# Kernel tuning notes

Measured on AMD Instinct MI355X. Metric: run time of the kernel, lower is better.

Reference implementation:

```python
import jax, jax.numpy as jnp
import numpy as np
from functools import partial

B, S, H = 1, 2048, 1024
F, E, K = 2048, 8, 2


def setup_inputs() -> dict:
    key = jax.random.key(0)
    ks = jax.random.split(key, 7)
    x = jax.random.normal(ks[0], (B, S, H), dtype=jnp.float32)
    weights = jax.random.uniform(ks[1], (B * S, E), dtype=jnp.float32)
    top_weights = jax.random.uniform(ks[2], (B * S, K), dtype=jnp.float32)
    top_experts = jax.random.randint(ks[3], (B * S, K), 0, E).astype(jnp.int64)
    scale = 0.02  # keep activations in a sane range
    w1 = jax.random.normal(ks[4], (E, F, H), dtype=jnp.float32) * scale
    v1 = jax.random.normal(ks[5], (E, F, H), dtype=jnp.float32) * scale
    w2 = jax.random.normal(ks[6], (E, F, H), dtype=jnp.float32) * scale
    return {"x": x, "weights": weights, "top_weights": top_weights,
            "top_experts": top_experts, "w1": w1, "v1": v1, "w2": w2}


def _moe_forward(x, top_weights, top_experts, w1, v1, w2):
    b, s, h = x.shape
    xf = x.reshape(-1, h)  # [T, H]
    n_exp = w1.shape[0]
    # combine weight per (token, expert): sum over top-k slots routed to e
    onehot = jax.nn.one_hot(top_experts, n_exp, dtype=x.dtype)      # [T, K, E]
    cw = jnp.einsum('tk,tke->et', top_weights, onehot)              # [E, T]

    def body(acc, inputs):
        w1e, v1e, w2e, cwe = inputs  # [F,H], [F,H], [F,H], [T]
        gate = jax.nn.silu(xf @ w1e.T)       # [T, F]
        inter = gate * (xf @ v1e.T)          # GLU
        down = inter @ w2e                   # [T, H]
        return acc + cwe[:, None] * down, None

    out, _ = jax.lax.scan(body, jnp.zeros_like(xf), (w1, v1, w2, cw))
    return out.reshape(b, s, h)


def reference(x, weights, top_weights, top_experts, w1, v1, w2):
    # `weights` (full router probs) is accepted but unused, as in the original.
    return _moe_forward(x, top_weights, top_experts, w1, v1, w2)
```

## Files before the change

kernel.cpp:

```cpp
#include <hip/hip_runtime.h>
#include <hip/hip_bf16.h>


#define T_ 2048
#define H_ 1024
#define F_ 2048
#define E_ 8

#define SCAP 768
#define NSLOT (E_ * SCAP)
#define MAXT2 (NSLOT / 128)

typedef unsigned short u16;
typedef short s8v __attribute__((ext_vector_type(8)));
typedef float f4v __attribute__((ext_vector_type(4)));
typedef unsigned short u16x4 __attribute__((ext_vector_type(4)));

__device__ __forceinline__ u16 f2bf(float f) {
    union { float f; unsigned u; } v; v.f = f;
    unsigned r = v.u + 0x7FFF + ((v.u >> 16) & 1);
    return (u16)(r >> 16);
}
__device__ __forceinline__ unsigned pkbf(float a, float b) {
    __hip_bfloat162 h = __float22bfloat162_rn(make_float2(a, b));
    union { __hip_bfloat162 h; unsigned u; } c; c.h = h; return c.u;
}
__device__ __forceinline__ int4 cvt8(const float4 a, const float4 b) {
    int4 r; r.x = (int)pkbf(a.x, a.y); r.y = (int)pkbf(a.z, a.w);
    r.z = (int)pkbf(b.x, b.y); r.w = (int)pkbf(b.z, b.w); return r;
}
__device__ __forceinline__ void async16(void* lds, const void* g) {
    __builtin_amdgcn_global_load_lds(
        (const __attribute__((address_space(1))) unsigned*)g,
        (__attribute__((address_space(3))) unsigned*)lds, 16, 0, 0);
}

__global__ void router_kernel(const int* __restrict__ te, const float* __restrict__ tw,
                              int* __restrict__ slot_tok, float* __restrict__ slot_w,
                              int* __restrict__ tok_slot,
                              int* __restrict__ tile_e, int* __restrict__ tile_s,
                              int* __restrict__ ntiles) {
    __shared__ int cnt[E_];
    __shared__ int s_any;
    int tid = threadIdx.x;
    if (tid < E_) cnt[tid] = 0;
    if (tid == 0) s_any = 0;
    __syncthreads();
    int any = 0;
    for (int i = tid; i < 2 * T_; i += 256) if (i & 1) any |= te[i];
    if (any) atomicOr(&s_any, 1);
    __syncthreads();
    bool is32 = (s_any != 0);
    for (int t = tid; t < T_; t += 256) {
        int e0 = is32 ? te[2 * t]     : te[4 * t];
        int e1 = is32 ? te[2 * t + 1] : te[4 * t + 2];
        float w0 = tw[2 * t], w1 = tw[2 * t + 1];
        if (e0 == e1) {
            int p = atomicAdd(&cnt[e0], 1);
            int s = (p < SCAP) ? e0 * SCAP + p : -1;
            if (s >= 0) { slot_tok[s] = t; slot_w[s] = w0 + w1; }
            tok_slot[2 * t] = s; tok_slot[2 * t + 1] = -1;
        } else {
            int p = atomicAdd(&cnt[e0], 1);
            int s = (p < SCAP) ? e0 * SCAP + p : -1;
            if (s >= 0) { slot_tok[s] = t; slot_w[s] = w0; }
            tok_slot[2 * t] = s;
            p = atomicAdd(&cnt[e1], 1);
            s = (p < SCAP) ? e1 * SCAP + p : -1;
            if (s >= 0) { slot_tok[s] = t; slot_w[s] = w1; }
            tok_slot[2 * t + 1] = s;
        }
    }
    __syncthreads();
    for (int e = 0; e < E_; ++e) {
        int c = min(cnt[e], SCAP);
        int pc = min((c + 127) & ~127, SCAP);
        for (int p = c + tid; p < pc; p += 256) {
            slot_tok[e * SCAP + p] = -1; slot_w[e * SCAP + p] = 0.f;
        }
    }
    __syncthreads();
    if (tid == 0) {
        int nt = 0;
        for (int e = 0; e < E_; ++e) {
            int pc = min((min(cnt[e], SCAP) + 127) & ~127, SCAP);
            for (int s = 0; s < pc; s += 128) { tile_e[nt] = e; tile_s[nt] = e * SCAP + s; ++nt; }
        }
        *ntiles = nt;
    }
}

__global__ void cvtwv_kernel(const float* __restrict__ w1, const float* __restrict__ v1,
                             u16* __restrict__ w1b, u16* __restrict__ v1b) {
    const float* src = blockIdx.y ? v1 : w1;
    u16* dst = blockIdx.y ? v1b : w1b;
    int i = (blockIdx.x * 256 + threadIdx.x) * 8;
    float4 a = *(const float4*)(src + i);
    float4 b = *(const float4*)(src + i + 4);
    *(int4*)(dst + i) = cvt8(a, b);
}

__global__ void tcvt8_kernel(const float* __restrict__ src0, u16* __restrict__ dst0) {
    const float* src = src0 + (size_t)blockIdx.z * F_ * H_;
    u16* dst = dst0 + (size_t)blockIdx.z * H_ * F_;
    __shared__ __align__(16) u16 tile[64][72];
    int bc = blockIdx.x * 64, br = blockIdx.y * 64;
    int tx = threadIdx.x, ty = threadIdx.y;
    for (int r = ty; r < 64; r += 32) {
        const float* p = src + (size_t)(br + r) * H_ + bc + tx * 8;
        float4 v0 = *(const float4*)p;
        float4 v1 = *(const float4*)(p + 4);
        u16* q = &tile[r][tx * 8];
        q[0] = f2bf(v0.x); q[1] = f2bf(v0.y); q[2] = f2bf(v0.z); q[3] = f2bf(v0.w);
        q[4] = f2bf(v1.x); q[5] = f2bf(v1.y); q[6] = f2bf(v1.z); q[7] = f2bf(v1.w);
    }
    __syncthreads();
    for (int c = ty; c < 64; c += 32) {
        u16 tmp[8];
#pragma unroll
        for (int j = 0; j < 8; ++j) tmp[j] = tile[tx * 8 + j][c];
        *(int4*)&dst[(size_t)(bc + c) * F_ + br + tx * 8] = *(int4*)tmp;
    }
}

__global__ void gather_x_kernel(const float* __restrict__ x, const int* __restrict__ slot_tok,
                                const int* __restrict__ tile_s, const int* __restrict__ ntiles,
                                u16* __restrict__ xg) {
    if ((int)blockIdx.x >= *ntiles) return;
    int base = tile_s[blockIdx.x];
    int tid = threadIdx.x;
    __shared__ int stok[128];
    if (tid < 128) stok[tid] = slot_tok[base + tid];
    __syncthreads();
    int c0 = blockIdx.y * 2048;
    for (int c = c0 + tid; c < c0 + 2048; c += 256) {
        int r = c >> 7, co = (c & 127) * 8;
        int tok = stok[r];
        u16* dst = xg + ((size_t)(base + r) << 10) + co;
        if (tok < 0) { *(int4*)dst = make_int4(0, 0, 0, 0); }
        else {
            const float* p = x + ((size_t)tok << 10) + co;
            *(int4*)dst = cvt8(*(const float4*)p, *(const float4*)(p + 4));
        }
    }
}

__global__ __launch_bounds__(256, 4) void glu_async_kernel(
        const u16* __restrict__ xg, const u16* __restrict__ w1b,
        const u16* __restrict__ v1b, const int* __restrict__ tile_e,
        const int* __restrict__ tile_s, const int* __restrict__ ntiles,
        const float* __restrict__ slot_w, u16* __restrict__ inter) {
    int bt = blockIdx.y;
    if (bt >= *ntiles) return;
    int e = tile_e[bt], s0 = tile_s[bt];
    int f0 = blockIdx.x * 64;
    __shared__ __align__(16) u16 As[2][128 * 32];
    __shared__ __align__(16) u16 B1s[2][64 * 32];
    __shared__ __align__(16) u16 B2s[2][64 * 32];
    __shared__ float swv[128];
    int tid = threadIdx.x;
    int lane = tid & 63, wave = tid >> 6;
    int wm = wave >> 1, wn = wave & 1;
    int ml = lane & 15, q = lane >> 4;
    if (tid < 128) swv[tid] = slot_w[s0 + tid];

    int row0 = (wave << 4) + (lane >> 2);
    int row1 = row0 + 64;
    int cs = ((lane & 3) ^ ((row0 >> 1) & 3)) << 3;
    const u16* gA0  = xg + ((size_t)(s0 + row0) << 10) + cs;
    const u16* gA1  = xg + ((size_t)(s0 + row1) << 10) + cs;
    const size_t wofs = (size_t)e * F_ * H_;
    const u16* gB1 = w1b + wofs + ((size_t)(f0 + row0) << 10) + cs;
    const u16* gB2 = v1b + wofs + ((size_t)(f0 + row0) << 10) + cs;
    int l0 = (row0 << 5) + ((lane & 3) << 3);
    int l1 = (row1 << 5) + ((lane & 3) << 3);
    int xs = (q ^ ((lane >> 1) & 3)) << 3;

    f4v accg[4][2] = {};
    f4v accu[4][2] = {};

    async16(&As[0][l0],  gA0);
    async16(&As[0][l1],  gA1);
    async16(&B1s[0][l0], gB1);
    async16(&B2s[0][l0], gB2);

    int cur = 0;
    for (int k0 = 0; k0 < H_; k0 += 32) {
        __syncthreads();
        if (k0 + 32 < H_) {
            int nx = cur ^ 1;
            async16(&As[nx][l0],  gA0 + k0 + 32);
            async16(&As[nx][l1],  gA1 + k0 + 32);
            async16(&B1s[nx][l0], gB1 + k0 + 32);
            async16(&B2s[nx][l0], gB2 + k0 + 32);
        }
        s8v a[4], b1[2], b2[2];
#pragma unroll
        for (int i = 0; i < 4; ++i)
            a[i]  = *(const s8v*)(&As[cur][(wm * 64 + i * 16 + ml) * 32 + xs]);
#pragma unroll
        for (int j = 0; j < 2; ++j) {
            b1[j] = *(const s8v*)(&B1s[cur][(wn * 32 + j * 16 + ml) * 32 + xs]);
            b2[j] = *(const s8v*)(&B2s[cur][(wn * 32 + j * 16 + ml) * 32 + xs]);
        }
#pragma unroll
        for (int i = 0; i < 4; ++i)
#pragma unroll
            for (int j = 0; j < 2; ++j) {
                accg[i][j] = __builtin_amdgcn_mfma_f32_16x16x32_bf16(a[i], b1[j], accg[i][j], 0, 0, 0);
                accu[i][j] = __builtin_amdgcn_mfma_f32_16x16x32_bf16(a[i], b2[j], accu[i][j], 0, 0, 0);
            }
        cur ^= 1;
    }
#pragma unroll
    for (int i = 0; i < 4; ++i)
#pragma unroll
        for (int r = 0; r < 4; ++r) {
            int lr = wm * 64 + i * 16 + q * 4 + r;
            float cv = swv[lr];
#pragma unroll
            for (int j = 0; j < 2; ++j) {
                float g = accg[i][j][r];
                float u = accu[i][j][r];
                float s = g / (1.f + __expf(-g));
                int f = f0 + wn * 32 + j * 16 + ml;
                inter[((size_t)(s0 + lr) << 11) + f] = f2bf(cv * s * u);
            }
        }
}

__global__ __launch_bounds__(256, 4) void down_async_kernel(
        const u16* __restrict__ inter, const u16* __restrict__ w2bT,
        const int* __restrict__ tile_e, const int* __restrict__ tile_s,
        const int* __restrict__ ntiles,
        float* __restrict__ dbufA, float* __restrict__ dbufB) {
    int bt = blockIdx.y;
    if (bt >= *ntiles) return;
    int e = tile_e[bt], s0 = tile_s[bt];
    int h0 = blockIdx.x * 64;
    int ks = blockIdx.z;
    int kbeg = ks * (F_ / 2);
    float* dbuf = ks ? dbufB : dbufA;
    __shared__ __align__(16) u16 As[2][128 * 32];
    __shared__ __align__(16) u16 Bs[2][64 * 32];
    int tid = threadIdx.x;
    int lane = tid & 63, wave = tid >> 6;
    int wm = wave >> 1, wn = wave & 1;
    int ml = lane & 15, q = lane >> 4;

    int row0 = (wave << 4) + (lane >> 2);
    int row1 = row0 + 64;
    int cs = ((lane & 3) ^ ((row0 >> 1) & 3)) << 3;
    const u16* gA0 = inter + ((size_t)(s0 + row0) << 11) + kbeg + cs;
    const u16* gA1 = inter + ((size_t)(s0 + row1) << 11) + kbeg + cs;
    const u16* gB  = w2bT + (size_t)e * H_ * F_ + ((size_t)(h0 + row0) << 11) + kbeg + cs;
    int l0 = (row0 << 5) + ((lane & 3) << 3);
    int l1 = (row1 << 5) + ((lane & 3) << 3);
    int xs = (q ^ ((lane >> 1) & 3)) << 3;

    f4v acc[4][2] = {};

    async16(&As[0][l0], gA0);
    async16(&As[0][l1], gA1);
    async16(&Bs[0][l0], gB);

    int cur = 0;
    for (int k0 = 0; k0 < F_ / 2; k0 += 32) {
        __syncthreads();
        if (k0 + 32 < F_ / 2) {
            int nx = cur ^ 1;
            async16(&As[nx][l0], gA0 + k0 + 32);
            async16(&As[nx][l1], gA1 + k0 + 32);
            async16(&Bs[nx][l0], gB  + k0 + 32);
        }
        s8v a[4], b[2];
#pragma unroll
        for (int i = 0; i < 4; ++i)
            a[i] = *(const s8v*)(&As[cur][(wm * 64 + i * 16 + ml) * 32 + xs]);
#pragma unroll
        for (int j = 0; j < 2; ++j)
            b[j] = *(const s8v*)(&Bs[cur][(wn * 32 + j * 16 + ml) * 32 + xs]);
#pragma unroll
        for (int i = 0; i < 4; ++i)
#pragma unroll
            for (int j = 0; j < 2; ++j)
                acc[i][j] = __builtin_amdgcn_mfma_f32_16x16x32_bf16(a[i], b[j], acc[i][j], 0, 0, 0);
        cur ^= 1;
    }
#pragma unroll
    for (int i = 0; i < 4; ++i)
#pragma unroll
        for (int r = 0; r < 4; ++r) {
            int lr = wm * 64 + i * 16 + q * 4 + r;
            float* drow = dbuf + ((size_t)(s0 + lr) << 10);
#pragma unroll
            for (int j = 0; j < 2; ++j) {
                int h = h0 + wn * 32 + j * 16 + ml;
                drow[h] = acc[i][j][r];
            }
        }
}

__global__ void combine_kernel(const float* __restrict__ dbufA, const float* __restrict__ dbufB,
                               const int* __restrict__ tok_slot, float* __restrict__ out) {
    int t = blockIdx.x;
    int c = threadIdx.x * 4;
    int s0 = tok_slot[2 * t], s1 = tok_slot[2 * t + 1];
    float4 acc = make_float4(0.f, 0.f, 0.f, 0.f);
    if (s0 >= 0) {
        float4 a = *(const float4*)(dbufA + ((size_t)s0 << 10) + c);
        float4 b = *(const float4*)(dbufB + ((size_t)s0 << 10) + c);
        acc.x = a.x + b.x; acc.y = a.y + b.y; acc.z = a.z + b.z; acc.w = a.w + b.w;
    }
    if (s1 >= 0) {
        float4 a = *(const float4*)(dbufA + ((size_t)s1 << 10) + c);
        float4 b = *(const float4*)(dbufB + ((size_t)s1 << 10) + c);
        acc.x += a.x + b.x; acc.y += a.y + b.y; acc.z += a.z + b.z; acc.w += a.w + b.w;
    }
    *(float4*)(out + ((size_t)t << 10) + c) = acc;
}

#define SCAP3 1024
__global__ void router3_kernel(const int* __restrict__ te, const float* __restrict__ tw,
                               int* __restrict__ cnt_g, int* __restrict__ slot_tok,
                               float* __restrict__ slot_w) {
    __shared__ int cnt[E_];
    __shared__ int s_any;
    int tid = threadIdx.x;
    if (tid < E_) cnt[tid] = 0;
    if (tid == 0) s_any = 0;
    __syncthreads();
    int any = 0;
    for (int i = tid; i < 2 * T_; i += 256) if (i & 1) any |= te[i];
    if (any) atomicOr(&s_any, 1);
    __syncthreads();
    bool is32 = (s_any != 0);
    for (int t = tid; t < T_; t += 256) {
        int e0 = is32 ? te[2 * t]     : te[4 * t];
        int e1 = is32 ? te[2 * t + 1] : te[4 * t + 2];
        float w0 = tw[2 * t], w1 = tw[2 * t + 1];
        if (e0 == e1) {
            int p = atomicAdd(&cnt[e0], 1);
            if (p < SCAP3) { slot_tok[e0 * SCAP3 + p] = t; slot_w[e0 * SCAP3 + p] = w0 + w1; }
        } else {
            int p = atomicAdd(&cnt[e0], 1);
            if (p < SCAP3) { slot_tok[e0 * SCAP3 + p] = t; slot_w[e0 * SCAP3 + p] = w0; }
            p = atomicAdd(&cnt[e1], 1);
            if (p < SCAP3) { slot_tok[e1 * SCAP3 + p] = t; slot_w[e1 * SCAP3 + p] = w1; }
        }
    }
    __syncthreads();
    for (int e = 0; e < E_; ++e) {
        int c = min(cnt[e], SCAP3);
        int pc = min((c + 127) & ~127, SCAP3);
        for (int p = c + tid; p < pc; p += 256) {
            slot_tok[e * SCAP3 + p] = 0; slot_w[e * SCAP3 + p] = 0.f;
        }
    }
    if (tid < E_) cnt_g[tid] = min(cnt[tid], SCAP3);
}
__global__ void cvt_kernel(const float* __restrict__ src, u16* __restrict__ dst) {
    int i = (blockIdx.x * 256 + threadIdx.x) * 4;
    float4 v = *(const float4*)(src + i);
    u16x4 o = { f2bf(v.x), f2bf(v.y), f2bf(v.z), f2bf(v.w) };
    *(u16x4*)(dst + i) = o;
}
__global__ __launch_bounds__(256, 2) void glu3_kernel(
        const u16* __restrict__ xb, const float* __restrict__ w1,
        const float* __restrict__ v1, const int* __restrict__ cnt_g,
        const int* __restrict__ slot_tok, const float* __restrict__ slot_w,
        u16* __restrict__ inter) {
    int e = blockIdx.x >> 3, tt = blockIdx.x & 7;
    if (tt * 128 >= cnt_g[e]) return;
    __shared__ __align__(16) u16 As[128 * 32];
    __shared__ __align__(16) u16 B1s[128 * 32];
    __shared__ __align__(16) u16 B2s[128 * 32];
    __shared__ int stok[128];
    __shared__ float sw[128];
    int tid = threadIdx.x;
    if (tid < 128) {
        stok[tid] = slot_tok[e * SCAP3 + tt * 128 + tid];
        sw[tid]   = slot_w[e * SCAP3 + tt * 128 + tid];
    }
    __syncthreads();
    int lane = tid & 63, wave = tid >> 6;
    int wm = wave >> 1, wn = wave & 1;
    int f0 = blockIdx.y * 128;
    int ml = lane & 15, q = lane >> 4;
    int r0 = tid >> 2, r1 = 64 + (tid >> 2);
    int colo = (tid & 3) * 8;
    const size_t tokoff0 = (size_t)stok[r0] * H_ + colo;
    const size_t tokoff1 = (size_t)stok[r1] * H_ + colo;
    const float* gb1 = w1 + (size_t)e * F_ * H_ + (size_t)f0 * H_;
    const float* gb2 = v1 + (size_t)e * F_ * H_ + (size_t)f0 * H_;
    const size_t boff0 = (size_t)r0 * H_ + colo;
    const size_t boff1 = (size_t)r1 * H_ + colo;
    f4v accg[4][4] = {};
    f4v accu[4][4] = {};
    for (int k0 = 0; k0 < H_; k0 += 32) {
        __syncthreads();
        *(int4*)(As + tid * 8)         = *(const int4*)(xb + tokoff0 + k0);
        *(int4*)(As + (256 + tid) * 8) = *(const int4*)(xb + tokoff1 + k0);
        const float* p = gb1 + boff0 + k0;
        *(int4*)(B1s + tid * 8) = cvt8(*(const float4*)p, *(const float4*)(p + 4));
        p = gb1 + boff1 + k0;
        *(int4*)(B1s + (256 + tid) * 8) = cvt8(*(const float4*)p, *(const float4*)(p + 4));
        p = gb2 + boff0 + k0;
        *(int4*)(B2s + tid * 8) = cvt8(*(const float4*)p, *(const float4*)(p + 4));
        p = gb2 + boff1 + k0;
        *(int4*)(B2s + (256 + tid) * 8) = cvt8(*(const float4*)p, *(const float4*)(p + 4));
        __syncthreads();
        s8v a[4], b1[4], b2[4];
#pragma unroll
        for (int i = 0; i < 4; ++i) {
            a[i]  = *(const s8v*)(As  + (wm * 64 + i * 16 + ml) * 32 + q * 8);
            b1[i] = *(const s8v*)(B1s + (wn * 64 + i * 16 + ml) * 32 + q * 8);
            b2[i] = *(const s8v*)(B2s + (wn * 64 + i * 16 + ml) * 32 + q * 8);
        }
#pragma unroll
        for (int i = 0; i < 4; ++i)
#pragma unroll
            for (int j = 0; j < 4; ++j) {
                accg[i][j] = __builtin_amdgcn_mfma_f32_16x16x32_bf16(a[i], b1[j], accg[i][j], 0, 0, 0);
                accu[i][j] = __builtin_amdgcn_mfma_f32_16x16x32_bf16(a[i], b2[j], accu[i][j], 0, 0, 0);
            }
    }
#pragma unroll
    for (int i = 0; i < 4; ++i)
#pragma unroll
        for (int r = 0; r < 4; ++r) {
            int lr = wm * 64 + i * 16 + q * 4 + r;
            float cv = sw[lr];
#pragma unroll
            for (int j = 0; j < 4; ++j) {
                float g = accg[i][j][r];
                float u = accu[i][j][r];
                float s = g / (1.f + __expf(-g));
                int f = f0 + wn * 64 + j * 16 + ml;
                inter[(size_t)(e * SCAP3 + tt * 128 + lr) * F_ + f] = f2bf(cv * s * u);
            }
        }
}
__global__ __launch_bounds__(256) void down3_kernel(
        const u16* __restrict__ inter, const u16* __restrict__ w2bT,
        const int* __restrict__ cnt_g, const int* __restrict__ slot_tok,
        float* __restrict__ out) {
    int e = blockIdx.x >> 3, tt = blockIdx.x & 7;
    if (tt * 128 >= cnt_g[e]) return;
    __shared__ __align__(16) u16 As[128 * 32];
    __shared__ __align__(16) u16 Bs[128 * 32];
    __shared__ int stok[128];
    int tid = threadIdx.x;
    if (tid < 128) stok[tid] = slot_tok[e * SCAP3 + tt * 128 + tid];
    __syncthreads();
    int lane = tid & 63, wave = tid >> 6;
    int wm = wave >> 1, wn = wave & 1;
    int h0 = blockIdx.y * 128;
    int ml = lane & 15, q = lane >> 4;
    int kbeg = blockIdx.z * (F_ / 2), kend = kbeg + (F_ / 2);
    f4v acc[4][4] = {};
    const u16* ga = inter + (size_t)(e * SCAP3 + tt * 128) * F_;
    const u16* gb = w2bT + (size_t)e * H_ * F_ + (size_t)h0 * F_;
    for (int k0 = kbeg; k0 < kend; k0 += 32) {
        __syncthreads();
#pragma unroll
        for (int p = 0; p < 2; ++p) {
            int c = p * 256 + tid;
            int r = c >> 2, co = (c & 3) * 8;
            *(int4*)(As + c * 8) = *(const int4*)(ga + (size_t)r * F_ + k0 + co);
            *(int4*)(Bs + c * 8) = *(const int4*)(gb + (size_t)r * F_ + k0 + co);
        }
        __syncthreads();
        s8v a[4], b[4];
#pragma unroll
        for (int i = 0; i < 4; ++i) {
            a[i] = *(const s8v*)(As + (wm * 64 + i * 16 + ml) * 32 + q * 8);
            b[i] = *(const s8v*)(Bs + (wn * 64 + i * 16 + ml) * 32 + q * 8);
        }
#pragma unroll
        for (int i = 0; i < 4; ++i)
#pragma unroll
            for (int j = 0; j < 4; ++j)
                acc[i][j] = __builtin_amdgcn_mfma_f32_16x16x32_bf16(a[i], b[j], acc[i][j], 0, 0, 0);
    }
#pragma unroll
    for (int i = 0; i < 4; ++i)
#pragma unroll
        for (int r = 0; r < 4; ++r) {
            int lr = wm * 64 + i * 16 + q * 4 + r;
            size_t trow = (size_t)stok[lr] * H_;
#pragma unroll
            for (int j = 0; j < 4; ++j) {
                int h = h0 + wn * 64 + j * 16 + ml;
                atomicAdd(&out[trow + h], acc[i][j][r]);
            }
        }
}

extern "C" void kernel_launch(void* const* d_in, const int* in_sizes, int n_in,
                              void* d_out, int out_size, void* d_ws, size_t ws_size,
                              hipStream_t stream) {
    const float* x  = (const float*)d_in[0];
    const float* tw = (const float*)d_in[2];
    const int*   te = (const int*)d_in[3];
    const float* w1 = (const float*)d_in[4];
    const float* v1 = (const float*)d_in[5];
    const float* w2 = (const float*)d_in[6];
    float* out = (float*)d_out;
    char* ws = (char*)d_ws;

    if (ws_size >= ((size_t)135 << 20)) {
        int*   ntiles   = (int*)(ws);
        int*   tile_e   = (int*)(ws + 256);
        int*   tile_s   = (int*)(ws + 512);
        int*   tok_slot = (int*)(ws + (4 << 10));
        int*   slot_tok = (int*)(ws + (20 << 10));
        float* slot_w   = (float*)(ws + (44 << 10));
        u16*   xg       = (u16*)(ws + ((size_t)1 << 20));
        u16*   w1b      = (u16*)(ws + ((size_t)13 << 20));
        u16*   v1b      = (u16*)(ws + ((size_t)45 << 20));
        u16*   w2bT     = (u16*)(ws + ((size_t)77 << 20));
        u16*   inter    = (u16*)(ws + ((size_t)109 << 20));
        float* dbufA    = (float*)(ws + ((size_t)13 << 20));
        float* dbufB    = (float*)(ws + ((size_t)45 << 20));

        router_kernel<<<1, 256, 0, stream>>>(te, tw, slot_tok, slot_w, tok_slot,
                                             tile_e, tile_s, ntiles);
        cvtwv_kernel<<<dim3((E_ * F_ * H_) / 2048, 2), 256, 0, stream>>>(w1, v1, w1b, v1b);
        tcvt8_kernel<<<dim3(H_ / 64, F_ / 64, E_), dim3(8, 32), 0, stream>>>(w2, w2bT);
        gather_x_kernel<<<dim3(MAXT2, 8), 256, 0, stream>>>(x, slot_tok, tile_s, ntiles, xg);
        glu_async_kernel<<<dim3(F_ / 64, MAXT2), 256, 0, stream>>>(
            xg, w1b, v1b, tile_e, tile_s, ntiles, slot_w, inter);
        down_async_kernel<<<dim3(H_ / 64, MAXT2, 2), 256, 0, stream>>>(
            inter, w2bT, tile_e, tile_s, ntiles, dbufA, dbufB);
        combine_kernel<<<T_, 256, 0, stream>>>(dbufA, dbufB, tok_slot, out);
    } else {
        int*   cnt_g    = (int*)(ws);
        int*   slot_tok = (int*)(ws + (4 << 10));
        float* slot_w   = (float*)(ws + (64 << 10));
        u16*   xb       = (u16*)(ws + ((size_t)1 << 20));
        u16*   w2bT     = (u16*)(ws + ((size_t)5 << 20));
        u16*   inter    = (u16*)(ws + ((size_t)37 << 20));

        hipMemsetAsync(out, 0, (size_t)T_ * H_ * sizeof(float), stream);
        router3_kernel<<<1, 256, 0, stream>>>(te, tw, cnt_g, slot_tok, slot_w);
        cvt_kernel<<<(T_ * H_) / 1024, 256, 0, stream>>>(x, xb);
        tcvt8_kernel<<<dim3(H_ / 64, F_ / 64, E_), dim3(8, 32), 0, stream>>>(w2, w2bT);
        glu3_kernel<<<dim3(E_ * 8, F_ / 128), 256, 0, stream>>>(
            xb, w1, v1, cnt_g, slot_tok, slot_w, inter);
        down3_kernel<<<dim3(E_ * 8, H_ / 128, 2), 256, 0, stream>>>(
            inter, w2bT, cnt_g, slot_tok, out);
    }
}
```

Before: 338.5 us.

## Triple-buffer GEMM async loads with explicit vmcnt waits; grid-stride weight conversion

Both the GLU and down-projection GEMM kernels move from double to triple buffering of their LDS tiles. They issue async loads two k-steps ahead and use explicit s_waitcnt vmcnt counts with raw barriers instead of __syncthreads. The goal is to hide more global-load latency behind MFMA work, at the cost of 50% more LDS per block, with the GLU occupancy hint lowered from 4 to 3. The w1/v1 bf16 conversion kernel becomes a grid-stride loop over a fixed 2048-block grid to cut launch and block-scheduling overhead.

After: 358.6 us. +5.9%, slower.

```diff
diff --git a/kernel.cpp b/kernel.cpp
--- a/kernel.cpp
+++ b/kernel.cpp
@@ -94,10 +94,13 @@
                              u16* __restrict__ w1b, u16* __restrict__ v1b) {
     const float* src = blockIdx.y ? v1 : w1;
     u16* dst = blockIdx.y ? v1b : w1b;
-    int i = (blockIdx.x * 256 + threadIdx.x) * 8;
-    float4 a = *(const float4*)(src + i);
-    float4 b = *(const float4*)(src + i + 4);
-    *(int4*)(dst + i) = cvt8(a, b);
+    const int total = E_ * F_ * H_;
+    const int stride = 2048 * 256 * 8;
+    for (int i = ((int)blockIdx.x * 256 + (int)threadIdx.x) * 8; i < total; i += stride) {
+        float4 a = *(const float4*)(src + i);
+        float4 b = *(const float4*)(src + i + 4);
+        *(int4*)(dst + i) = cvt8(a, b);
+    }
 }
 
 __global__ void tcvt8_kernel(const float* __restrict__ src0, u16* __restrict__ dst0) {
@@ -145,7 +148,7 @@
     }
 }
 
-__global__ __launch_bounds__(256, 4) void glu_async_kernel(
+__global__ __launch_bounds__(256, 3) void glu_async_kernel(
         const u16* __restrict__ xg, const u16* __restrict__ w1b,
         const u16* __restrict__ v1b, const int* __restrict__ tile_e,
         const int* __restrict__ tile_s, const int* __restrict__ ntiles,
@@ -154,9 +157,9 @@
     if (bt >= *ntiles) return;
     int e = tile_e[bt], s0 = tile_s[bt];
     int f0 = blockIdx.x * 64;
-    __shared__ __align__(16) u16 As[2][128 * 32];
-    __shared__ __align__(16) u16 B1s[2][64 * 32];
-    __shared__ __align__(16) u16 B2s[2][64 * 32];
+    __shared__ __align__(16) u16 As[3][128 * 32];
+    __shared__ __align__(16) u16 B1s[3][64 * 32];
+    __shared__ __align__(16) u16 B2s[3][64 * 32];
     __shared__ float swv[128];
     int tid = threadIdx.x;
     int lane = tid & 63, wave = tid >> 6;
@@ -179,29 +182,32 @@
     f4v accg[4][2] = {};
     f4v accu[4][2] = {};
 
-    async16(&As[0][l0],  gA0);
-    async16(&As[0][l1],  gA1);
-    async16(&B1s[0][l0], gB1);
-    async16(&B2s[0][l0], gB2);
-
-    int cur = 0;
-    for (int k0 = 0; k0 < H_; k0 += 32) {
-        __syncthreads();
-        if (k0 + 32 < H_) {
-            int nx = cur ^ 1;
-            async16(&As[nx][l0],  gA0 + k0 + 32);
-            async16(&As[nx][l1],  gA1 + k0 + 32);
-            async16(&B1s[nx][l0], gB1 + k0 + 32);
-            async16(&B2s[nx][l0], gB2 + k0 + 32);
-        }
+#define GLU_ISSUE(t, b) do { int _k = (t) << 5;                      \
+        async16(&As[b][l0],  gA0 + _k);                              \
+        async16(&As[b][l1],  gA1 + _k);                              \
+        async16(&B1s[b][l0], gB1 + _k);                              \
+        async16(&B2s[b][l0], gB2 + _k); } while (0)
+
+    GLU_ISSUE(0, 0);
+    GLU_ISSUE(1, 1);
+    const int NT = H_ / 32;
+    int cb = 0, nb = 2;
+    for (int t = 0; t < NT; ++t) {
+        if (t < NT - 1) asm volatile("s_waitcnt vmcnt(4)" ::: "memory");
+        else            asm volatile("s_waitcnt vmcnt(0)" ::: "memory");
+        __builtin_amdgcn_s_barrier();
+        if (t + 2 < NT) GLU_ISSUE(t + 2, nb);
+        const u16* Ab  = As[cb];
+        const u16* B1b = B1s[cb];
+        const u16* B2b = B2s[cb];
         s8v a[4], b1[2], b2[2];
 #pragma unroll
         for (int i = 0; i < 4; ++i)
-            a[i]  = *(const s8v*)(&As[cur][(wm * 64 + i * 16 + ml) * 32 + xs]);
+            a[i]  = *(const s8v*)(Ab + (wm * 64 + i * 16 + ml) * 32 + xs);
 #pragma unroll
         for (int j = 0; j < 2; ++j) {
-            b1[j] = *(const s8v*)(&B1s[cur][(wn * 32 + j * 16 + ml) * 32 + xs]);
-            b2[j] = *(const s8v*)(&B2s[cur][(wn * 32 + j * 16 + ml) * 32 + xs]);
+            b1[j] = *(const s8v*)(B1b + (wn * 32 + j * 16 + ml) * 32 + xs);
+            b2[j] = *(const s8v*)(B2b + (wn * 32 + j * 16 + ml) * 32 + xs);
         }
 #pragma unroll
         for (int i = 0; i < 4; ++i)
@@ -210,8 +216,10 @@
                 accg[i][j] = __builtin_amdgcn_mfma_f32_16x16x32_bf16(a[i], b1[j], accg[i][j], 0, 0, 0);
                 accu[i][j] = __builtin_amdgcn_mfma_f32_16x16x32_bf16(a[i], b2[j], accu[i][j], 0, 0, 0);
             }
-        cur ^= 1;
-    }
+        int cn = cb + 1; cb = (cn == 3) ? 0 : cn;
+        cn = nb + 1; nb = (cn == 3) ? 0 : cn;
+    }
+#undef GLU_ISSUE
 #pragma unroll
     for (int i = 0; i < 4; ++i)
 #pragma unroll
@@ -241,8 +249,8 @@
     int ks = blockIdx.z;
     int kbeg = ks * (F_ / 2);
     float* dbuf = ks ? dbufB : dbufA;
-    __shared__ __align__(16) u16 As[2][128 * 32];
-    __shared__ __align__(16) u16 Bs[2][64 * 32];
+    __shared__ __align__(16) u16 As[3][128 * 32];
+    __shared__ __align__(16) u16 Bs[3][64 * 32];
     int tid = threadIdx.x;
     int lane = tid & 63, wave = tid >> 6;
     int wm = wave >> 1, wn = wave & 1;
@@ -260,33 +268,38 @@
 
     f4v acc[4][2] = {};
 
-    async16(&As[0][l0], gA0);
-    async16(&As[0][l1], gA1);
-    async16(&Bs[0][l0], gB);
-
-    int cur = 0;
-    for (int k0 = 0; k0 < F_ / 2; k0 += 32) {
-        __syncthreads();
-        if (k0 + 32 < F_ / 2) {
-            int nx = cur ^ 1;
-            async16(&As[nx][l0], gA0 + k0 + 32);
-            async16(&As[nx][l1], gA1 + k0 + 32);
-            async16(&Bs[nx][l0], gB  + k0 + 32);
-        }
+#define DWN_ISSUE(t, b) do { int _k = (t) << 5;                      \
+        async16(&As[b][l0], gA0 + _k);                               \
+        async16(&As[b][l1], gA1 + _k);                               \
+        async16(&Bs[b][l0], gB  + _k); } while (0)
+
+    DWN_ISSUE(0, 0);
+    DWN_ISSUE(1, 1);
+    const int NT = (F_ / 2) / 32;
+    int cb = 0, nb = 2;
+    for (int t = 0; t < NT; ++t) {
+        if (t < NT - 1) asm volatile("s_waitcnt vmcnt(3)" ::: "memory");
+        else            asm volatile("s_waitcnt vmcnt(0)" ::: "memory");
+        __builtin_amdgcn_s_barrier();
+        if (t + 2 < NT) DWN_ISSUE(t + 2, nb);
+        const u16* Ab = As[cb];
+        const u16* Bb = Bs[cb];
         s8v a[4], b[2];
 #pragma unroll
         for (int i = 0; i < 4; ++i)
-            a[i] = *(const s8v*)(&As[cur][(wm * 64 + i * 16 + ml) * 32 + xs]);
+            a[i] = *(const s8v*)(Ab + (wm * 64 + i * 16 + ml) * 32 + xs);
 #pragma unroll
         for (int j = 0; j < 2; ++j)
-            b[j] = *(const s8v*)(&Bs[cur][(wn * 32 + j * 16 + ml) * 32 + xs]);
+            b[j] = *(const s8v*)(Bb + (wn * 32 + j * 16 + ml) * 32 + xs);
 #pragma unroll
         for (int i = 0; i < 4; ++i)
 #pragma unroll
             for (int j = 0; j < 2; ++j)
                 acc[i][j] = __builtin_amdgcn_mfma_f32_16x16x32_bf16(a[i], b[j], acc[i][j], 0, 0, 0);
-        cur ^= 1;
-    }
+        int cn = cb + 1; cb = (cn == 3) ? 0 : cn;
+        cn = nb + 1; nb = (cn == 3) ? 0 : cn;
+    }
+#undef DWN_ISSUE
 #pragma unroll
     for (int i = 0; i < 4; ++i)
 #pragma unroll
@@ -526,7 +539,7 @@
 
         router_kernel<<<1, 256, 0, stream>>>(te, tw, slot_tok, slot_w, tok_slot,
                                              tile_e, tile_s, ntiles);
-        cvtwv_kernel<<<dim3((E_ * F_ * H_) / 2048, 2), 256, 0, stream>>>(w1, v1, w1b, v1b);
+        cvtwv_kernel<<<dim3(2048, 2), 256, 0, stream>>>(w1, v1, w1b, v1b);
         tcvt8_kernel<<<dim3(H_ / 64, F_ / 64, E_), dim3(8, 32), 0, stream>>>(w2, w2bT);
         gather_x_kernel<<<dim3(MAXT2, 8), 256, 0, stream>>>(x, slot_tok, tile_s, ntiles, xg);
         glu_async_kernel<<<dim3(F_ / 64, MAXT2), 256, 0, stream>>>(
```

## Fuse w1/v1 fp32-to-bf16 conversion into GLU kernel B-tile loads

Applied to the files above, without the earlier changes.

Drops the separate pass that converted w1 and v1 to bf16 in the workspace. The GLU kernel now loads fp32 weights into registers, converts them while staging into swizzled LDS, and prefetches the next K slice into registers. This removes a full read and write of both weight tensors. In exchange, every token tile re-reads the fp32 weights, at twice the bytes of bf16, which raises GLU-kernel memory traffic and register use.

Result: faster. 324.1 us (-4.3%).

```diff
diff --git a/kernel.cpp b/kernel.cpp
--- a/kernel.cpp
+++ b/kernel.cpp
@@ -90,16 +90,6 @@
     }
 }
 
-__global__ void cvtwv_kernel(const float* __restrict__ w1, const float* __restrict__ v1,
-                             u16* __restrict__ w1b, u16* __restrict__ v1b) {
-    const float* src = blockIdx.y ? v1 : w1;
-    u16* dst = blockIdx.y ? v1b : w1b;
-    int i = (blockIdx.x * 256 + threadIdx.x) * 8;
-    float4 a = *(const float4*)(src + i);
-    float4 b = *(const float4*)(src + i + 4);
-    *(int4*)(dst + i) = cvt8(a, b);
-}
-
 __global__ void tcvt8_kernel(const float* __restrict__ src0, u16* __restrict__ dst0) {
     const float* src = src0 + (size_t)blockIdx.z * F_ * H_;
     u16* dst = dst0 + (size_t)blockIdx.z * H_ * F_;
@@ -146,8 +136,8 @@
 }
 
 __global__ __launch_bounds__(256, 4) void glu_async_kernel(
-        const u16* __restrict__ xg, const u16* __restrict__ w1b,
-        const u16* __restrict__ v1b, const int* __restrict__ tile_e,
+        const u16* __restrict__ xg, const float* __restrict__ w1,
+        const float* __restrict__ v1, const int* __restrict__ tile_e,
         const int* __restrict__ tile_s, const int* __restrict__ ntiles,
         const float* __restrict__ slot_w, u16* __restrict__ inter) {
     int bt = blockIdx.y;
@@ -169,30 +159,43 @@
     int cs = ((lane & 3) ^ ((row0 >> 1) & 3)) << 3;
     const u16* gA0  = xg + ((size_t)(s0 + row0) << 10) + cs;
     const u16* gA1  = xg + ((size_t)(s0 + row1) << 10) + cs;
-    const size_t wofs = (size_t)e * F_ * H_;
-    const u16* gB1 = w1b + wofs + ((size_t)(f0 + row0) << 10) + cs;
-    const u16* gB2 = v1b + wofs + ((size_t)(f0 + row0) << 10) + cs;
     int l0 = (row0 << 5) + ((lane & 3) << 3);
     int l1 = (row1 << 5) + ((lane & 3) << 3);
+
+    int brow = tid >> 2;
+    int bc   = tid & 3;
+    const size_t wofs = (size_t)e * F_ * H_;
+    const float* gB1 = w1 + wofs + (size_t)(f0 + brow) * H_ + bc * 8;
+    const float* gB2 = v1 + wofs + (size_t)(f0 + brow) * H_ + bc * 8;
+    int lb = (brow << 5) + ((bc ^ ((brow >> 1) & 3)) << 3);
+
     int xs = (q ^ ((lane >> 1) & 3)) << 3;
 
     f4v accg[4][2] = {};
     f4v accu[4][2] = {};
 
-    async16(&As[0][l0],  gA0);
-    async16(&As[0][l1],  gA1);
-    async16(&B1s[0][l0], gB1);
-    async16(&B2s[0][l0], gB2);
-
+    float4 rb1a = *(const float4*)(gB1);
+    float4 rb1b = *(const float4*)(gB1 + 4);
+    float4 rb2a = *(const float4*)(gB2);
+    float4 rb2b = *(const float4*)(gB2 + 4);
+    async16(&As[0][l0], gA0);
+    async16(&As[0][l1], gA1);
+
+    const int NT = H_ / 32;
     int cur = 0;
-    for (int k0 = 0; k0 < H_; k0 += 32) {
+    for (int t = 0; t < NT; ++t) {
+        *(int4*)(&B1s[cur][lb]) = cvt8(rb1a, rb1b);
+        *(int4*)(&B2s[cur][lb]) = cvt8(rb2a, rb2b);
         __syncthreads();
-        if (k0 + 32 < H_) {
+        if (t + 1 < NT) {
+            int k = (t + 1) << 5;
+            rb1a = *(const float4*)(gB1 + k);
+            rb1b = *(const float4*)(gB1 + k + 4);
+            rb2a = *(const float4*)(gB2 + k);
+            rb2b = *(const float4*)(gB2 + k + 4);
             int nx = cur ^ 1;
-            async16(&As[nx][l0],  gA0 + k0 + 32);
-            async16(&As[nx][l1],  gA1 + k0 + 32);
-            async16(&B1s[nx][l0], gB1 + k0 + 32);
-            async16(&B2s[nx][l0], gB2 + k0 + 32);
+            async16(&As[nx][l0], gA0 + k);
+            async16(&As[nx][l1], gA1 + k);
         }
         s8v a[4], b1[2], b2[2];
 #pragma unroll
@@ -517,8 +520,6 @@
         int*   slot_tok = (int*)(ws + (20 << 10));
         float* slot_w   = (float*)(ws + (44 << 10));
         u16*   xg       = (u16*)(ws + ((size_t)1 << 20));
-        u16*   w1b      = (u16*)(ws + ((size_t)13 << 20));
-        u16*   v1b      = (u16*)(ws + ((size_t)45 << 20));
         u16*   w2bT     = (u16*)(ws + ((size_t)77 << 20));
         u16*   inter    = (u16*)(ws + ((size_t)109 << 20));
         float* dbufA    = (float*)(ws + ((size_t)13 << 20));
@@ -526,11 +527,10 @@
 
         router_kernel<<<1, 256, 0, stream>>>(te, tw, slot_tok, slot_w, tok_slot,
                                              tile_e, tile_s, ntiles);
-        cvtwv_kernel<<<dim3((E_ * F_ * H_) / 2048, 2), 256, 0, stream>>>(w1, v1, w1b, v1b);
         tcvt8_kernel<<<dim3(H_ / 64, F_ / 64, E_), dim3(8, 32), 0, stream>>>(w2, w2bT);
         gather_x_kernel<<<dim3(MAXT2, 8), 256, 0, stream>>>(x, slot_tok, tile_s, ntiles, xg);
         glu_async_kernel<<<dim3(F_ / 64, MAXT2), 256, 0, stream>>>(
-            xg, w1b, v1b, tile_e, tile_s, ntiles, slot_w, inter);
+            xg, w1, v1, tile_e, tile_s, ntiles, slot_w, inter);
         down_async_kernel<<<dim3(H_ / 64, MAXT2, 2), 256, 0, stream>>>(
             inter, w2bT, tile_e, tile_s, ntiles, dbufA, dbufB);
         combine_kernel<<<T_, 256, 0, stream>>>(dbufA, dbufB, tok_slot, out);
```
